# Performance work log

Measured on AMD Instinct MI355X. Metric: run time of the kernel, lower is better.

The kernel has to match this reference:

```python
import jax, jax.numpy as jnp
import numpy as np

NGRAMS = (1, 2, 3, 4)


def _conv1d(x, W, b):
    # x: [B, S, E], W: [D, E, K], b: [D] -> [B, S-K+1, D] (valid conv, torch Conv1d)
    y = jax.lax.conv_general_dilated(
        x.transpose(0, 2, 1), W, window_strides=(1,), padding='VALID',
        dimension_numbers=('NCH', 'OIH', 'NCH'))
    return y.transpose(0, 2, 1) + b


def setup_inputs() -> dict:
    key = jax.random.key(0)
    ks = jax.random.split(key, 9)
    B, S, E, D = 64, 512, 256, 512
    inp = {'features': jax.random.normal(ks[0], (B, S, E), dtype=jnp.float32)}
    for i, n in enumerate(NGRAMS):
        fan_in = E * n
        inp[f'W{n}'] = jax.random.normal(ks[1 + 2 * i], (D, E, n), dtype=jnp.float32) / np.sqrt(fan_in)
        inp[f'b{n}'] = jax.random.normal(ks[2 + 2 * i], (D,), dtype=jnp.float32) * 0.01
    return inp


def reference(features, W1, b1, W2, b2, W3, b3, W4, b4):
    Ws = (W1, W2, W3, W4)
    bs = (b1, b2, b3, b4)
    # n-gram conv branches: branch g has kernel size NGRAMS[g] = g+1, length S - g
    feats = [_conv1d(features, W, b) for W, b in zip(Ws, bs)]
    B, S, E = features.shape
    flen = E  # faithful to original: features_len = features.shape[-1] (the embed dim)
    out = feats[0]  # unigram features, [B, S, D]
    i = jnp.arange(flen)
    add = jnp.zeros((B, flen, out.shape[-1]), out.dtype)
    # Original nested loops: out[:, i] += sum_{g=1}^{maxn-1} sum_{p=max(0,i-g+1)}^{min(i+1,L_g)-1} feats[g][:, p]
    # Computed here with per-branch prefix sums (exclusive) -> windowed sums.
    for g in range(1, max(NGRAMS)):
        y = feats[g]                      # [B, L, D], L = S - g
        L = y.shape[1]
        P = jnp.concatenate([jnp.zeros_like(y[:, :1]), jnp.cumsum(y, axis=1)], axis=1)  # [B, L+1, D]
        hi = jnp.minimum(i + 1, L)
        lo = jnp.minimum(jnp.maximum(0, i - g + 1), L)
        win = P[:, hi] - P[:, lo]         # [B, flen, D]
        add = add + jnp.where((hi > lo)[None, :, None], win, jnp.zeros_like(win))
    return out.at[:, :flen].add(add)
```

## Files before the change

kernel.cpp:

```cpp
#include <hip/hip_runtime.h>
#include <hip/hip_bf16.h>

#define EDIM 256
#define SDIM 512
#define BDIM 64
#define DDIM 512
#define SPAD 514

#define OFF_XP    0u
#define OFF_BFI   16842752u
#define OFF_BFT   18415616u
#define OFF_CORR  18677760u
#define OFF_BI    18939904u

#define CVT_BLOCKS  4112
#define WB_BASE     4112
#define CORR_BASE   4624
#define PREP_BLOCKS 8720

typedef __attribute__((ext_vector_type(8))) __bf16 bf16x8;
typedef __attribute__((ext_vector_type(4))) float  f32x4;
typedef __attribute__((ext_vector_type(8))) unsigned short ushort8v;

__device__ __forceinline__ unsigned short f2bf(float f) {
    unsigned int u = __float_as_uint(f);
    u = (u + 0x7fffu + ((u >> 16) & 1u)) >> 16;
    return (unsigned short)u;
}

__global__ __launch_bounds__(256) void prep_all(
    const float* __restrict__ X,
    const float* __restrict__ W1, const float* __restrict__ b1,
    const float* __restrict__ W2, const float* __restrict__ b2,
    const float* __restrict__ W3, const float* __restrict__ b3,
    const float* __restrict__ W4, const float* __restrict__ b4,
    char* __restrict__ wsb)
{
    const int tid = threadIdx.x;

    if (blockIdx.x < CVT_BLOCKS) {
        unsigned short* Xp = (unsigned short*)(wsb + OFF_XP);
        const int i   = blockIdx.x * 256 + tid;
        const int row = i >> 5;
        const int q   = i & 31;
        const int b   = row / SPAD;
        const int j   = row - b * SPAD;
        ushort8v v;
        if (j < 2) {
            v = (ushort8v)0;
        } else {
            const float* src = X + ((size_t)(b * SDIM + j - 2)) * EDIM + q * 8;
            const float4 f0 = *(const float4*)(src);
            const float4 f1 = *(const float4*)(src + 4);
            v[0] = f2bf(f0.x); v[1] = f2bf(f0.y); v[2] = f2bf(f0.z); v[3] = f2bf(f0.w);
            v[4] = f2bf(f1.x); v[5] = f2bf(f1.y); v[6] = f2bf(f1.z); v[7] = f2bf(f1.w);
        }
        *(ushort8v*)(Xp + (size_t)row * EDIM + q * 8) = v;
        return;
    }

    if (blockIdx.x < CORR_BASE) {
        const int d = blockIdx.x - WB_BASE;
        const int e = tid;
        const int de = d * EDIM + e;

        const float w1  = W1[de];
        const float w20 = W2[de * 2 + 0], w21 = W2[de * 2 + 1];
        const float w30 = W3[de * 3 + 0], w31 = W3[de * 3 + 1], w32 = W3[de * 3 + 2];
        const float w40 = W4[de * 4 + 0], w41 = W4[de * 4 + 1], w42 = W4[de * 4 + 2], w43 = W4[de * 4 + 3];

        float g[6];
        g[0] = w40;
        g[1] = w30 + w40 + w41;
        g[2] = w1 + w20 + w30 + w31 + w40 + w41 + w42;
        g[3] = w21 + w31 + w32 + w41 + w42 + w43;
        g[4] = w32 + w42 + w43;
        g[5] = w43;

        const int fm = d & 15, t = (d >> 4) & 3, h = (d >> 6) & 1, c = d >> 7;
        const int hi = (e >> 3) & 3, j = e & 7, eb = e >> 5;
        char* ibase = wsb + OFF_BFI + (size_t)((c * 2 + h) * 48) * 4096
                    + t * 1024 + hi * 256 + fm * 16 + j * 2;
#pragma unroll
        for (int s = 0; s < 6; ++s)
            *(unsigned short*)(ibase + (size_t)(s * 8 + eb) * 4096) = f2bf(g[s]);

        *(unsigned short*)(wsb + OFF_BFT + (size_t)((c * 2 + h) * 8 + eb) * 4096
                           + t * 1024 + hi * 256 + fm * 16 + j * 2) = f2bf(w1);

        if (e == 0)
            ((float*)(wsb + OFF_BI))[d] = b1[d] + b2[d] + 2.0f * b3[d] + 3.0f * b4[d];
        return;
    }

    {
        __shared__ float cls[16];
        const int cb = blockIdx.x - CORR_BASE;
        const int d  = cb >> 3;
        const int bq = (cb & 7) * 8;
        const int e  = tid;

        if (tid < 16) cls[tid] = 0.f;

        const float w31 = W3[(size_t)d * 768 + 3 * e + 1];
        const float w32 = W3[(size_t)d * 768 + 3 * e + 2];
        const float4 w4v = *(const float4*)(W4 + (size_t)d * 1024 + 4 * e);
        const float w41 = w4v.y, w42 = w4v.z, w43 = w4v.w;

        const float c00 = w31 + w41 + w42;
        const float c01 = w32 + w42 + w43;
        const float c02 = w43;
        __syncthreads();

#pragma unroll
        for (int bi = 0; bi < 8; ++bi) {
            const float* xr = X + (size_t)(bq + bi) * (SDIM * EDIM) + e;
            const float x0 = xr[0], x1 = xr[EDIM], x2 = xr[2 * EDIM];
            float a0 = c00 * x0 + c01 * x1 + c02 * x2;
            float a1 = w41 * x0 + w42 * x1 + w43 * x2;
#pragma unroll
            for (int off = 32; off >= 1; off >>= 1) {
                a0 += __shfl_xor(a0, off, 64);
                a1 += __shfl_xor(a1, off, 64);
            }
            if ((tid & 63) == 0) {
                atomicAdd(&cls[bi * 2 + 0], a0);
                atomicAdd(&cls[bi * 2 + 1], a1);
            }
        }
        __syncthreads();

        if (tid < 16) {
            const int s = tid & 1;
            const float bc = s ? b4[d] : (b3[d] + 2.f * b4[d]);
            ((float*)(wsb + OFF_CORR))[(size_t)d * 128 + bq * 2 + tid] = -cls[tid] - bc;
        }
    }
}

#define GLL(src, dst) \
    __builtin_amdgcn_global_load_lds((const __attribute__((address_space(1))) void*)(src), \
                                     (__attribute__((address_space(3))) void*)(dst), 16, 0, 0)

#define TSTRIDE 132

__global__ __launch_bounds__(512, 4) void mega(
    const unsigned short* __restrict__ Xp,
    const char* __restrict__ wsb,
    const float* __restrict__ b1,
    float* __restrict__ out)
{
    __shared__ __align__(16) char smem[67584];
    const int id  = blockIdx.x;
    const int strip = id & 127;
    const int c     = id >> 7;
    const int col0  = c * 128;
    const int tid = threadIdx.x;
    const int w = tid >> 6, l = tid & 63;

    const int swz = ((l & 7) ^ (l >> 3)) * 16;
    const int r0  = strip * 128 + 16 * w + (l >> 3);
    const int r1  = r0 + 8;
    const int ba0 = r0 >> 8, sa0 = r0 & 255;
    const int ba1 = r1 >> 8, sa1 = r1 & 255;

    const int oA0 = (16 * w) * 128;
    const int oA1 = oA0 + 1024;
    char* q0 = smem;
    char* q1 = smem + 16384;
    char* q2 = smem + 32768;
    char* q3 = smem + 49152;

    const int wrg = (w >> 2) * 64;
    const int qc  = w & 3;
    const int fm  = l & 15;
    const int hi4 = l >> 4;
    const int rs0 = ((hi4)     ^ (fm & 7)) * 16;
    const int rs1 = ((4 + hi4) ^ (fm & 7)) * 16;

    const int hq   = qc >> 1;
    const int toff = (qc & 1) * 2048;
    const char* bfi = wsb + OFF_BFI + (size_t)(c * 2 + hq) * (48 * 4096) + toff + l * 16;
    const char* bft = wsb + OFF_BFT + (size_t)(c * 2 + hq) * (8 * 4096)  + toff + l * 16;

    f32x4 acc[4][2];
    const char *ga0, *ga1;

    auto LOADB = [&](bf16x8 (&dst)[4], const char* base, int ph) {
#pragma unroll
        for (int ks = 0; ks < 2; ++ks)
#pragma unroll
            for (int j = 0; j < 2; ++j)
                dst[ks * 2 + j] = *(const bf16x8*)(base + (size_t)(2 * ph + ks) * 4096 + j * 1024);
    };
    auto STAGE = [&](char* buf) {
        GLL(ga0, buf + oA0);
        GLL(ga1, buf + oA1);
        ga0 += 128; ga1 += 128;
    };
    auto COMP = [&](const char* buf, const bf16x8 (&b)[4]) {
#pragma unroll
        for (int ks = 0; ks < 2; ++ks) {
            bf16x8 af[4];
            const int rs = ks ? rs1 : rs0;
#pragma unroll
            for (int t = 0; t < 4; ++t)
                af[t] = *(const bf16x8*)(buf + (wrg + t * 16 + fm) * 128 + rs);
#pragma unroll
            for (int i = 0; i < 4; ++i)
#pragma unroll
                for (int j = 0; j < 2; ++j)
                    acc[i][j] = __builtin_amdgcn_mfma_f32_16x16x32_bf16(af[i], b[ks * 2 + j], acc[i][j], 0, 0, 0);
        }
    };

#define PH6  asm volatile("s_waitcnt vmcnt(6) lgkmcnt(0)" ::: "memory"); \
             __builtin_amdgcn_s_barrier();
#define PH0  asm volatile("s_waitcnt vmcnt(0) lgkmcnt(0)" ::: "memory"); \
             __builtin_amdgcn_s_barrier();
#define DO_COMP(Q, B) __builtin_amdgcn_s_setprio(1); COMP(Q, B); __builtin_amdgcn_s_setprio(0);

    auto GEMM = [&](const char* bbase, int np) {
        bf16x8 b0[4], b1r[4], b2[4], b3[4];
        STAGE(q0); LOADB(b0,  bbase, 0);
        STAGE(q1); LOADB(b1r, bbase, 1);
#pragma unroll 1
        for (int p = 0; p + 4 < np; p += 4) {
            PH6; STAGE(q2); LOADB(b2,  bbase, p + 2); DO_COMP(q0, b0);
            PH6; STAGE(q3); LOADB(b3,  bbase, p + 3); DO_COMP(q1, b1r);
            PH6; STAGE(q0); LOADB(b0,  bbase, p + 4); DO_COMP(q2, b2);
            PH6; STAGE(q1); LOADB(b1r, bbase, p + 5); DO_COMP(q3, b3);
        }
        PH6; STAGE(q2); LOADB(b2, bbase, np - 2); DO_COMP(q0, b0);
        PH6; STAGE(q3); LOADB(b3, bbase, np - 1); DO_COMP(q1, b1r);
        PH6;                                      DO_COMP(q2, b2);
        PH0;                                      DO_COMP(q3, b3);
    };

    auto EPI = [&](int s_base, bool with_corr) {
        const float* bias = with_corr ? (const float*)(wsb + OFF_BI) : b1;
        const float* corr = (const float*)(wsb + OFF_CORR);
        const int ocol = col0 + qc * 32 + fm;
        const int rq   = hi4 * 4;
        float bv[2];
#pragma unroll
        for (int j = 0; j < 2; ++j) bv[j] = bias[ocol + j * 16];

        float* T = (float*)smem;
#pragma unroll
        for (int i = 0; i < 4; ++i) {
#pragma unroll
            for (int r = 0; r < 4; ++r) {
                const int row = wrg + i * 16 + rq + r;
                const int rr  = strip * 128 + row;
                const int ssl = rr & 255;
                const int bb  = rr >> 8;
#pragma unroll
                for (int j = 0; j < 2; ++j) {
                    float v = acc[i][j][r] + bv[j];
                    if (with_corr && ssl < 2)
                        v += corr[(size_t)(ocol + j * 16) * 128 + bb * 2 + ssl];
                    T[row * TSTRIDE + qc * 32 + j * 16 + fm] = v;
                }
            }
        }
        asm volatile("s_waitcnt lgkmcnt(0)" ::: "memory");
        __builtin_amdgcn_s_barrier();
        const int c16   = l & 31;
        const int rhalf = l >> 5;
#pragma unroll
        for (int itr = 0; itr < 8; ++itr) {
            const int row = w * 16 + 2 * itr + rhalf;
            const f32x4 v = *(const f32x4*)(T + row * TSTRIDE + c16 * 4);
            const int rr  = strip * 128 + row;
            const int ssl = rr & 255;
            const int bb  = rr >> 8;
            float* op = out + ((size_t)(bb * SDIM + s_base + ssl)) * DDIM + col0 + c16 * 4;
            __builtin_nontemporal_store(v, (f32x4*)op);
        }
        asm volatile("s_waitcnt lgkmcnt(0)" ::: "memory");
        __builtin_amdgcn_s_barrier();
    };

#pragma unroll
    for (int i = 0; i < 4; ++i)
#pragma unroll
        for (int j = 0; j < 2; ++j) acc[i][j] = (f32x4){0.f, 0.f, 0.f, 0.f};
    ga0 = (const char*)(Xp + (size_t)(ba0 * SPAD + sa0) * EDIM) + swz;
    ga1 = (const char*)(Xp + (size_t)(ba1 * SPAD + sa1) * EDIM) + swz;
    GEMM(bfi, 24);
    EPI(0, true);

#pragma unroll
    for (int i = 0; i < 4; ++i)
#pragma unroll
        for (int j = 0; j < 2; ++j) acc[i][j] = (f32x4){0.f, 0.f, 0.f, 0.f};
    ga0 = (const char*)(Xp + (size_t)(ba0 * SPAD + 258 + sa0) * EDIM) + swz;
    ga1 = (const char*)(Xp + (size_t)(ba1 * SPAD + 258 + sa1) * EDIM) + swz;
    GEMM(bft, 4);
    EPI(256, false);
}

extern "C" void kernel_launch(void* const* d_in, const int* in_sizes, int n_in,
                              void* d_out, int out_size, void* d_ws, size_t ws_size,
                              hipStream_t stream)
{
    const float* X  = (const float*)d_in[0];
    const float* W1 = (const float*)d_in[1];
    const float* b1 = (const float*)d_in[2];
    const float* W2 = (const float*)d_in[3];
    const float* b2 = (const float*)d_in[4];
    const float* W3 = (const float*)d_in[5];
    const float* b3 = (const float*)d_in[6];
    const float* W4 = (const float*)d_in[7];
    const float* b4 = (const float*)d_in[8];
    float* out = (float*)d_out;
    char*  wsb = (char*)d_ws;

    prep_all<<<dim3(PREP_BLOCKS), dim3(256), 0, stream>>>(X, W1, b1, W2, b2, W3, b3, W4, b4, wsb);

    mega<<<dim3(512), dim3(512), 0, stream>>>(
        (const unsigned short*)(wsb + OFF_XP), wsb, b1, out);
}
```

Before: 161.1 us.

## Fuse fp32-to-bf16 input conversion into GEMM A-tile loading

```diff
diff --git a/kernel.cpp b/kernel.cpp
--- a/kernel.cpp
+++ b/kernel.cpp
@@ -3,20 +3,16 @@
 
 #define EDIM 256
 #define SDIM 512
-#define BDIM 64
 #define DDIM 512
-#define SPAD 514
-
-#define OFF_XP    0u
-#define OFF_BFI   16842752u
-#define OFF_BFT   18415616u
-#define OFF_CORR  18677760u
-#define OFF_BI    18939904u
-
-#define CVT_BLOCKS  4112
-#define WB_BASE     4112
-#define CORR_BASE   4624
-#define PREP_BLOCKS 8720
+
+#define OFF_BFI   0u
+#define OFF_BFT   1572864u
+#define OFF_CORR  1835008u
+#define OFF_BI    2097152u
+#define OFF_ZERO  2099200u
+
+#define WB_BLOCKS   512
+#define PREP_BLOCKS 4608
 
 typedef __attribute__((ext_vector_type(8))) __bf16 bf16x8;
 typedef __attribute__((ext_vector_type(4))) float  f32x4;
@@ -38,31 +34,13 @@
 {
     const int tid = threadIdx.x;
 
-    if (blockIdx.x < CVT_BLOCKS) {
-        unsigned short* Xp = (unsigned short*)(wsb + OFF_XP);
-        const int i   = blockIdx.x * 256 + tid;
-        const int row = i >> 5;
-        const int q   = i & 31;
-        const int b   = row / SPAD;
-        const int j   = row - b * SPAD;
-        ushort8v v;
-        if (j < 2) {
-            v = (ushort8v)0;
-        } else {
-            const float* src = X + ((size_t)(b * SDIM + j - 2)) * EDIM + q * 8;
-            const float4 f0 = *(const float4*)(src);
-            const float4 f1 = *(const float4*)(src + 4);
-            v[0] = f2bf(f0.x); v[1] = f2bf(f0.y); v[2] = f2bf(f0.z); v[3] = f2bf(f0.w);
-            v[4] = f2bf(f1.x); v[5] = f2bf(f1.y); v[6] = f2bf(f1.z); v[7] = f2bf(f1.w);
-        }
-        *(ushort8v*)(Xp + (size_t)row * EDIM + q * 8) = v;
-        return;
-    }
-
-    if (blockIdx.x < CORR_BASE) {
-        const int d = blockIdx.x - WB_BASE;
+    if (blockIdx.x < WB_BLOCKS) {
+        const int d = blockIdx.x;
         const int e = tid;
         const int de = d * EDIM + e;
+
+        if (blockIdx.x == 0)
+            *(float4*)(wsb + OFF_ZERO + tid * 16) = make_float4(0.f, 0.f, 0.f, 0.f);
 
         const float w1  = W1[de];
         const float w20 = W2[de * 2 + 0], w21 = W2[de * 2 + 1];
@@ -95,7 +73,7 @@
 
     {
         __shared__ float cls[16];
-        const int cb = blockIdx.x - CORR_BASE;
+        const int cb = blockIdx.x - WB_BLOCKS;
         const int d  = cb >> 3;
         const int bq = (cb & 7) * 8;
         const int e  = tid;
@@ -138,14 +116,10 @@
     }
 }
 
-#define GLL(src, dst) \
-    __builtin_amdgcn_global_load_lds((const __attribute__((address_space(1))) void*)(src), \
-                                     (__attribute__((address_space(3))) void*)(dst), 16, 0, 0)
-
 #define TSTRIDE 132
 
 __global__ __launch_bounds__(512, 4) void mega(
-    const unsigned short* __restrict__ Xp,
+    const float* __restrict__ X,
     const char* __restrict__ wsb,
     const float* __restrict__ b1,
     float* __restrict__ out)
@@ -158,18 +132,16 @@
     const int tid = threadIdx.x;
     const int w = tid >> 6, l = tid & 63;
 
-    const int swz = ((l & 7) ^ (l >> 3)) * 16;
-    const int r0  = strip * 128 + 16 * w + (l >> 3);
-    const int r1  = r0 + 8;
-    const int ba0 = r0 >> 8, sa0 = r0 & 255;
-    const int ba1 = r1 >> 8, sa1 = r1 & 255;
-
-    const int oA0 = (16 * w) * 128;
-    const int oA1 = oA0 + 1024;
     char* q0 = smem;
     char* q1 = smem + 16384;
     char* q2 = smem + 32768;
     char* q3 = smem + 49152;
+
+    const int rbase = strip * 128 + 16 * w + (l >> 3);
+    const int bb0  = rbase >> 8;
+    const int ssl0 = rbase & 255;
+    const int qm_int = 2 - ssl0;
+    const int wrow = (16 * w + (l >> 3)) * 128 + ((l & 7) ^ (l >> 3)) * 16;
 
     const int wrg = (w >> 2) * 64;
     const int qc  = w & 3;
@@ -182,6 +154,7 @@
     const int toff = (qc & 1) * 2048;
     const char* bfi = wsb + OFF_BFI + (size_t)(c * 2 + hq) * (48 * 4096) + toff + l * 16;
     const char* bft = wsb + OFF_BFT + (size_t)(c * 2 + hq) * (8 * 4096)  + toff + l * 16;
+    const char* zb  = wsb + OFF_ZERO + (l & 7) * 32;
 
     f32x4 acc[4][2];
     const char *ga0, *ga1;
@@ -193,10 +166,25 @@
             for (int j = 0; j < 2; ++j)
                 dst[ks * 2 + j] = *(const bf16x8*)(base + (size_t)(2 * ph + ks) * 4096 + j * 1024);
     };
-    auto STAGE = [&](char* buf) {
-        GLL(ga0, buf + oA0);
-        GLL(ga1, buf + oA1);
-        ga0 += 128; ga1 += 128;
+    auto LOADA = [&](f32x4 (&d)[4], int p, int qm) {
+        const char* s0 = ((p >> 2) >= qm) ? ga0 : zb;
+        d[0] = *(const f32x4*)(s0);
+        d[1] = *(const f32x4*)(s0 + 16);
+        d[2] = *(const f32x4*)(ga1);
+        d[3] = *(const f32x4*)(ga1 + 16);
+        ga0 += 256; ga1 += 256;
+    };
+    auto WRA = [&](const f32x4 (&a)[4], char* buf) {
+        ushort8v u0, u1;
+#pragma unroll
+        for (int j = 0; j < 4; ++j) {
+            u0[j]     = f2bf(a[0][j]);
+            u0[4 + j] = f2bf(a[1][j]);
+            u1[j]     = f2bf(a[2][j]);
+            u1[4 + j] = f2bf(a[3][j]);
+        }
+        *(ushort8v*)(buf + wrow)        = u0;
+        *(ushort8v*)(buf + wrow + 1024) = u1;
     };
     auto COMP = [&](const char* buf, const bf16x8 (&b)[4]) {
 #pragma unroll
@@ -214,30 +202,40 @@
         }
     };
 
-#define PH6  asm volatile("s_waitcnt vmcnt(6) lgkmcnt(0)" ::: "memory"); \
-             __builtin_amdgcn_s_barrier();
-#define PH0  asm volatile("s_waitcnt vmcnt(0) lgkmcnt(0)" ::: "memory"); \
-             __builtin_amdgcn_s_barrier();
+#define VM8   asm volatile("s_waitcnt vmcnt(8)" ::: "memory");
+#define VM0   asm volatile("s_waitcnt vmcnt(0)" ::: "memory");
+#define LK0B  asm volatile("s_waitcnt lgkmcnt(0)" ::: "memory"); __builtin_amdgcn_s_barrier();
 #define DO_COMP(Q, B) __builtin_amdgcn_s_setprio(1); COMP(Q, B); __builtin_amdgcn_s_setprio(0);
 
-    auto GEMM = [&](const char* bbase, int np) {
-        bf16x8 b0[4], b1r[4], b2[4], b3[4];
-        STAGE(q0); LOADB(b0,  bbase, 0);
-        STAGE(q1); LOADB(b1r, bbase, 1);
+    auto GEMM = [&](const char* bbase, int np, int qm) {
+        bf16x8 B0[4], B1[4], B2[4], B3[4];
+        f32x4 Aev[4], Aod[4];
+        LOADA(Aev, 0, qm); LOADB(B0, bbase, 0);
+        LOADA(Aod, 1, qm); LOADB(B1, bbase, 1);
+        VM8;
+        WRA(Aev, q0);
+        LK0B;
 #pragma unroll 1
         for (int p = 0; p + 4 < np; p += 4) {
-            PH6; STAGE(q2); LOADB(b2,  bbase, p + 2); DO_COMP(q0, b0);
-            PH6; STAGE(q3); LOADB(b3,  bbase, p + 3); DO_COMP(q1, b1r);
-            PH6; STAGE(q0); LOADB(b0,  bbase, p + 4); DO_COMP(q2, b2);
-            PH6; STAGE(q1); LOADB(b1r, bbase, p + 5); DO_COMP(q3, b3);
-        }
-        PH6; STAGE(q2); LOADB(b2, bbase, np - 2); DO_COMP(q0, b0);
-        PH6; STAGE(q3); LOADB(b3, bbase, np - 1); DO_COMP(q1, b1r);
-        PH6;                                      DO_COMP(q2, b2);
-        PH0;                                      DO_COMP(q3, b3);
+            LOADA(Aev, p + 2, qm); LOADB(B2, bbase, p + 2);
+            VM8; WRA(Aod, q1); LK0B; DO_COMP(q0, B0);
+            LOADA(Aod, p + 3, qm); LOADB(B3, bbase, p + 3);
+            VM8; WRA(Aev, q2); LK0B; DO_COMP(q1, B1);
+            LOADA(Aev, p + 4, qm); LOADB(B0, bbase, p + 4);
+            VM8; WRA(Aod, q3); LK0B; DO_COMP(q2, B2);
+            LOADA(Aod, p + 5, qm); LOADB(B1, bbase, p + 5);
+            VM8; WRA(Aev, q0); LK0B; DO_COMP(q3, B3);
+        }
+        LOADA(Aev, np - 2, qm); LOADB(B2, bbase, np - 2);
+        VM8; WRA(Aod, q1); LK0B; DO_COMP(q0, B0);
+        LOADA(Aod, np - 1, qm); LOADB(B3, bbase, np - 1);
+        VM8; WRA(Aev, q2); LK0B; DO_COMP(q1, B1);
+        VM0; WRA(Aod, q3); LK0B; DO_COMP(q2, B2);
+        DO_COMP(q3, B3);
     };
 
     auto EPI = [&](int s_base, bool with_corr) {
+        LK0B;
         const float* bias = with_corr ? (const float*)(wsb + OFF_BI) : b1;
         const float* corr = (const float*)(wsb + OFF_CORR);
         const int ocol = col0 + qc * 32 + fm;
@@ -264,8 +262,7 @@
                 }
             }
         }
-        asm volatile("s_waitcnt lgkmcnt(0)" ::: "memory");
-        __builtin_amdgcn_s_barrier();
+        LK0B;
         const int c16   = l & 31;
         const int rhalf = l >> 5;
 #pragma unroll
@@ -278,26 +275,25 @@
             float* op = out + ((size_t)(bb * SDIM + s_base + ssl)) * DDIM + col0 + c16 * 4;
             __builtin_nontemporal_store(v, (f32x4*)op);
         }
-        asm volatile("s_waitcnt lgkmcnt(0)" ::: "memory");
-        __builtin_amdgcn_s_barrier();
+        LK0B;
     };
 
 #pragma unroll
     for (int i = 0; i < 4; ++i)
 #pragma unroll
         for (int j = 0; j < 2; ++j) acc[i][j] = (f32x4){0.f, 0.f, 0.f, 0.f};
-    ga0 = (const char*)(Xp + (size_t)(ba0 * SPAD + sa0) * EDIM) + swz;
-    ga1 = (const char*)(Xp + (size_t)(ba1 * SPAD + sa1) * EDIM) + swz;
-    GEMM(bfi, 24);
+    ga0 = (const char*)(X + (ptrdiff_t)(bb0 * SDIM + ssl0 - 2) * EDIM + (l & 7) * 8);
+    ga1 = (const char*)(X + (ptrdiff_t)(bb0 * SDIM + ssl0 + 6) * EDIM + (l & 7) * 8);
+    GEMM(bfi, 24, qm_int);
     EPI(0, true);
 
 #pragma unroll
     for (int i = 0; i < 4; ++i)
 #pragma unroll
         for (int j = 0; j < 2; ++j) acc[i][j] = (f32x4){0.f, 0.f, 0.f, 0.f};
-    ga0 = (const char*)(Xp + (size_t)(ba0 * SPAD + 258 + sa0) * EDIM) + swz;
-    ga1 = (const char*)(Xp + (size_t)(ba1 * SPAD + 258 + sa1) * EDIM) + swz;
-    GEMM(bft, 4);
+    ga0 = (const char*)(X + (size_t)(bb0 * SDIM + 256 + ssl0) * EDIM + (l & 7) * 8);
+    ga1 = (const char*)(X + (size_t)(bb0 * SDIM + 264 + ssl0) * EDIM + (l & 7) * 8);
+    GEMM(bft, 4, -1000);
     EPI(256, false);
 }
 
@@ -319,6 +315,5 @@
 
     prep_all<<<dim3(PREP_BLOCKS), dim3(256), 0, stream>>>(X, W1, b1, W2, b2, W3, b3, W4, b4, wsb);
 
-    mega<<<dim3(512), dim3(512), 0, stream>>>(
-        (const unsigned short*)(wsb + OFF_XP), wsb, b1, out);
+    mega<<<dim3(512), dim3(512), 0, stream>>>(X, wsb, b1, out);
 }
```

Result: slower. 251.0 us (+55.7%).
